# Kernel tuning notes

Hardware: AMD Instinct MI355X
Metric: run time of the kernel (lower is better)

The kernel has to match this reference:

```python
import jax, jax.numpy as jnp
import numpy as np

B, T, E, D, A = 32, 2048, 1024, 1024, 1024
SHARPENING = 1.0


def setup_inputs() -> dict:
    key = jax.random.key(0)
    ks = jax.random.split(key, 8)
    s = 0.02
    return {
        "enc_out": jax.random.normal(ks[0], (B, T, E), jnp.float32),
        "x_lens": jax.random.randint(ks[1], (B,), 1, T + 1, jnp.int32),
        "dec_out": jax.random.normal(ks[2], (B, 1, D), jnp.float32),
        "att_weights_step": jax.random.uniform(ks[3], (B, T), jnp.float32),
        "W_enc": jax.random.normal(ks[4], (E, A), jnp.float32) * s,
        "b_enc": jnp.zeros((A,), jnp.float32),
        "W_dec": jax.random.normal(ks[5], (D, A), jnp.float32) * s,
        "v": jax.random.normal(ks[6], (A,), jnp.float32) * s,
    }


def reference(enc_out, x_lens, dec_out, att_weights_step, W_enc, b_enc, W_dec, v):
    # content (Bahdanau additive) attention
    # energy[b,t] = v . tanh(W_enc enc[b,t] + b_enc + W_dec dec[b])
    enc_proj = jnp.einsum("bte,ea->bta", enc_out, W_enc) + b_enc  # [B,T,A]
    dec_proj = jnp.einsum("bod,da->boa", dec_out, W_dec)          # [B,1,A]
    energy = jnp.einsum("bta,a->bt", jnp.tanh(enc_proj + dec_proj), v)  # [B,T]
    # original multiplies energy by a 0/1 length mask (NOT -inf masking)
    mask = (jnp.arange(T)[None, :] < x_lens[:, None]).astype(energy.dtype)
    energy = energy * mask * SHARPENING
    att = jax.nn.softmax(energy, axis=-1)  # [B,T]
    context_vec = jnp.einsum("bte,bt->be", enc_out, att)[:, None, :]  # [B,1,E]
    return context_vec, att
```

## Files before the change

kernel.cpp:

```cpp
#include <hip/hip_runtime.h>
#include <hip/hip_bf16.h>
#include <stdint.h>


typedef __bf16 bf16;
typedef __bf16 bf16x8 __attribute__((ext_vector_type(8)));
typedef __bf16 bf16x4 __attribute__((ext_vector_type(4)));
typedef float floatx4 __attribute__((ext_vector_type(4)));

#define T_DIM 2048
#define B_DIM 32
#define K_DIM 1024
#define N_DIM 1024
#define M_DIM (B_DIM * T_DIM)
#define ENC_ELEMS ((size_t)M_DIM * K_DIM)

__device__ __forceinline__ void async_copy16(const bf16* g, bf16* l) {
    __builtin_amdgcn_global_load_lds(
        (const __attribute__((address_space(1))) void*)g,
        (__attribute__((address_space(3))) void*)l, 16, 0, 0);
}

__device__ __forceinline__ float fast_tanh(float x) {
    float ax = fabsf(x);
    float e  = __expf(ax + ax);
    float t  = 1.f - 2.f / (e + 1.f);
    return copysignf(t, x);
}

__global__ __launch_bounds__(256) void cvt_enc(const float* __restrict__ in,
                                               bf16* __restrict__ out) {
    size_t i = ((size_t)blockIdx.x * 256 + threadIdx.x) * 8;
    const size_t stride = (size_t)gridDim.x * 256 * 8;
    for (; i < ENC_ELEMS; i += stride) {
        float4 f0 = *(const float4*)(in + i);
        float4 f1 = *(const float4*)(in + i + 4);
        bf16x8 w;
        w[0] = (bf16)f0.x; w[1] = (bf16)f0.y; w[2] = (bf16)f0.z; w[3] = (bf16)f0.w;
        w[4] = (bf16)f1.x; w[5] = (bf16)f1.y; w[6] = (bf16)f1.z; w[7] = (bf16)f1.w;
        *(bf16x8*)(out + i) = w;
    }
}

__global__ __launch_bounds__(256) void transpose_wenc(
        const float* __restrict__ W, bf16* __restrict__ WT) {
    __shared__ bf16 tile[64][65];
    const int e0 = blockIdx.x * 64, a0 = blockIdx.y * 64;
    const int c = threadIdx.x & 63, r0 = threadIdx.x >> 6;
#pragma unroll
    for (int p = 0; p < 16; ++p) {
        int r = p * 4 + r0;
        tile[r][c] = (bf16)W[(size_t)(e0 + r) * 1024 + a0 + c];
    }
    __syncthreads();
#pragma unroll
    for (int p = 0; p < 16; ++p) {
        int r = p * 4 + r0;
        WT[(size_t)(a0 + r) * 1024 + e0 + c] = tile[c][r];
    }
}

__global__ __launch_bounds__(256) void decproj_kernel(
        const float* __restrict__ dec, const float* __restrict__ Wdec,
        const float* __restrict__ benc, float* __restrict__ dproj) {
    const int bg = blockIdx.x;
    const int a0 = blockIdx.y * 64;
    const int al = threadIdx.x & 63;
    const int dq = threadIdx.x >> 6;
    const int a  = a0 + al;
    __shared__ float sdec[8][1024];
    for (int i = threadIdx.x; i < 8192; i += 256)
        sdec[i >> 10][i & 1023] = dec[bg * 8192 + i];
    __syncthreads();
    float acc[8];
#pragma unroll
    for (int b = 0; b < 8; ++b) acc[b] = 0.f;
    for (int d = dq * 256; d < dq * 256 + 256; ++d) {
        const float w = Wdec[(size_t)d * 1024 + a];
#pragma unroll
        for (int b = 0; b < 8; ++b) acc[b] += sdec[b][d] * w;
    }
    __shared__ float red[4][8][64];
#pragma unroll
    for (int b = 0; b < 8; ++b) red[dq][b][al] = acc[b];
    __syncthreads();
    if (dq == 0) {
        const float be = benc[a];
#pragma unroll
        for (int b = 0; b < 8; ++b)
            dproj[(bg * 8 + b) * 1024 + a] =
                be + red[0][b][al] + red[1][b][al] + red[2][b][al] + red[3][b][al];
    }
}


#define HT 8192

#define BARRIER()  __builtin_amdgcn_s_barrier()
#define SCHEDB()   __builtin_amdgcn_sched_barrier(0)
#define VMCNT(n)   asm volatile("s_waitcnt vmcnt(" #n ")")

#define STAGE_A(kt, h, sl) {                                                   \
    const bf16* g_ = encb + (size_t)(m0 + (h)*128 + wave*8 + (lane>>3)) * 1024 \
                     + (kt)*64 + srccol;                                       \
    bf16* l_ = As + (((sl)*2 + (h)) * HT) + wave * 512;                        \
    async_copy16(g_, l_);                                                      \
    async_copy16(g_ + (size_t)64*1024, l_ + 4096);                             \
}
#define STAGE_B(kt, h) {                                                       \
    const bf16* g_ = WT + (size_t)(n0 + (h)*128 + wave*8 + (lane>>3)) * 1024   \
                     + (kt)*64 + srccol;                                       \
    bf16* l_ = Bs + ((((kt)&1)*2 + (h)) * HT) + wave * 512;                    \
    async_copy16(g_, l_);                                                      \
    async_copy16(g_ + (size_t)64*1024, l_ + 4096);                             \
}

__global__ __launch_bounds__(512, 2) void energy_gemm_8ph(
        const bf16* __restrict__ encb, const bf16* __restrict__ WT,
        const float* __restrict__ dproj, const float* __restrict__ v,
        float* __restrict__ part) {
    __shared__ __align__(16) bf16 As[6 * HT];
    __shared__ __align__(16) bf16 Bs[4 * HT];
    float* esum = (float*)As;

    const int tid  = threadIdx.x;
    const int lane = tid & 63;
    const int wave = tid >> 6;
    const int wm   = wave >> 2;
    const int wn   = wave & 3;
    const int lo   = lane & 15;
    const int hi   = lane >> 4;

    const int L = blockIdx.x;
    const int xcd  = L & 7;
    const int slot = L >> 3;
    const int m_tile  = xcd * 32 + (slot >> 2);
    const int n_chunk = slot & 3;
    const int m0 = m_tile * 256;
    const int n0 = n_chunk * 256;
    const int b  = m0 >> 11;

    const int srccol = (((lane & 7) ^ (lane >> 3)) << 3);
    const int swz0 = ((hi)     ^ (lo & 7)) << 3;
    const int swz1 = ((4 | hi) ^ (lo & 7)) << 3;

    floatx4 acc[2][2][4][2];
#pragma unroll
    for (int a_ = 0; a_ < 2; ++a_)
#pragma unroll
      for (int b_ = 0; b_ < 2; ++b_)
#pragma unroll
        for (int c_ = 0; c_ < 4; ++c_)
#pragma unroll
          for (int d_ = 0; d_ < 2; ++d_)
            acc[a_][b_][c_][d_] = (floatx4){0.f, 0.f, 0.f, 0.f};

    float vv[2][2], dp[2][2];
#pragma unroll
    for (int qn = 0; qn < 2; ++qn)
#pragma unroll
      for (int nf = 0; nf < 2; ++nf) {
        int col = n0 + qn * 128 + wn * 32 + nf * 16 + lo;
        vv[qn][nf] = v[col];
        dp[qn][nf] = dproj[b * 1024 + col];
      }
    SCHEDB();
    VMCNT(0);
    SCHEDB();

    STAGE_B(0, 0); STAGE_B(0, 1);
    STAGE_A(0, 0, 0); STAGE_A(0, 1, 0);
    STAGE_A(1, 0, 1); STAGE_A(1, 1, 1);
    SCHEDB();
    VMCNT(4);
    SCHEDB();
    BARRIER();

    int aslot = 0;
#pragma unroll 1
    for (int t = 0; t < 16; ++t) {
        const int tb   = t & 1;
        const int asl2 = (aslot >= 1) ? (aslot - 1) : 2;
        const bf16* Bh0 = Bs + (tb * 2 + 0) * HT;
        const bf16* Bh1 = Bs + (tb * 2 + 1) * HT;
        const bf16* Ah0 = As + (aslot * 2 + 0) * HT;
        const bf16* Ah1 = As + (aslot * 2 + 1) * HT;

        bf16x8 bfr[2][2][2], af0[4][2], af1[4][2];
#pragma unroll
        for (int qn = 0; qn < 2; ++qn) {
            const bf16* Bh_ = qn ? Bh1 : Bh0;
#pragma unroll
            for (int nf = 0; nf < 2; ++nf) {
                bfr[qn][nf][0] = *(const bf16x8*)(Bh_ + (wn*32 + nf*16 + lo)*64 + swz0);
                bfr[qn][nf][1] = *(const bf16x8*)(Bh_ + (wn*32 + nf*16 + lo)*64 + swz1);
            }
        }
#pragma unroll
        for (int mf = 0; mf < 4; ++mf) {
            af0[mf][0] = *(const bf16x8*)(Ah0 + (wm*64 + mf*16 + lo)*64 + swz0);
            af0[mf][1] = *(const bf16x8*)(Ah0 + (wm*64 + mf*16 + lo)*64 + swz1);
        }
        if (t < 15) { STAGE_B(t + 1, 0); STAGE_B(t + 1, 1); }

        __builtin_amdgcn_s_setprio(1);
#pragma unroll
        for (int kk = 0; kk < 2; ++kk)
#pragma unroll
          for (int mf = 0; mf < 4; ++mf)
#pragma unroll
            for (int qn = 0; qn < 2; ++qn)
#pragma unroll
              for (int nf = 0; nf < 2; ++nf)
                acc[0][qn][mf][nf] = __builtin_amdgcn_mfma_f32_16x16x32_bf16(
                    af0[mf][kk], bfr[qn][nf][kk], acc[0][qn][mf][nf], 0, 0, 0);
        __builtin_amdgcn_s_setprio(0);

#pragma unroll
        for (int mf = 0; mf < 4; ++mf) {
            af1[mf][0] = *(const bf16x8*)(Ah1 + (wm*64 + mf*16 + lo)*64 + swz0);
            af1[mf][1] = *(const bf16x8*)(Ah1 + (wm*64 + mf*16 + lo)*64 + swz1);
        }
        if (t < 14) { STAGE_A(t + 2, 0, asl2); STAGE_A(t + 2, 1, asl2); }

        __builtin_amdgcn_s_setprio(1);
#pragma unroll
        for (int kk = 0; kk < 2; ++kk)
#pragma unroll
          for (int mf = 0; mf < 4; ++mf)
#pragma unroll
            for (int qn = 0; qn < 2; ++qn)
#pragma unroll
              for (int nf = 0; nf < 2; ++nf)
                acc[1][qn][mf][nf] = __builtin_amdgcn_mfma_f32_16x16x32_bf16(
                    af1[mf][kk], bfr[qn][nf][kk], acc[1][qn][mf][nf], 0, 0, 0);
        __builtin_amdgcn_s_setprio(0);

        SCHEDB();
        if (t < 14) { VMCNT(4); } else if (t == 14) { VMCNT(0); }
        SCHEDB();
        BARRIER();
        aslot = (aslot == 2) ? 0 : aslot + 1;
    }

    __syncthreads();
#pragma unroll
    for (int qm = 0; qm < 2; ++qm)
#pragma unroll
      for (int mf = 0; mf < 4; ++mf)
#pragma unroll
        for (int r = 0; r < 4; ++r) {
          float s = 0.f;
#pragma unroll
          for (int qn = 0; qn < 2; ++qn)
#pragma unroll
            for (int nf = 0; nf < 2; ++nf)
              s += vv[qn][nf] * fast_tanh(acc[qm][qn][mf][nf][r] + dp[qn][nf]);
          s += __shfl_xor(s, 1);
          s += __shfl_xor(s, 2);
          s += __shfl_xor(s, 4);
          s += __shfl_xor(s, 8);
          if (lo == 0)
            esum[wn * 256 + qm * 128 + wm * 64 + mf * 16 + hi * 4 + r] = s;
        }
    __syncthreads();
    if (tid < 256)
        part[(size_t)n_chunk * M_DIM + m0 + tid] =
            esum[tid] + esum[256 + tid] + esum[512 + tid] + esum[768 + tid];
}

__global__ __launch_bounds__(256) void energy_gemm_f32(
        const float* __restrict__ enc, const bf16* __restrict__ WT,
        const float* __restrict__ dproj, const float* __restrict__ v,
        float* __restrict__ part) {
    __shared__ __align__(16) bf16 As[128 * 32];
    __shared__ __align__(16) bf16 Bs[128 * 32];
    __shared__ float esum[128];

    const int tid  = threadIdx.x;
    const int lane = tid & 63;
    const int wave = tid >> 6;
    const int wy = wave >> 1, wx = wave & 1;
    const int L = blockIdx.x;
    const int xcd  = L & 7;
    const int slot = L >> 3;
    const int m_tile = xcd * 64 + (slot >> 3);
    const int n_chunk = slot & 7;
    const int m0 = m_tile * 128;
    const int n0 = n_chunk * 128;
    const int b  = m0 >> 11;

    if (tid < 128) esum[tid] = 0.f;

    floatx4 acc[4][4];
#pragma unroll
    for (int i = 0; i < 4; ++i)
#pragma unroll
        for (int j = 0; j < 4; ++j) acc[i][j] = (floatx4){0.f, 0.f, 0.f, 0.f};

    const int sr = tid >> 2;
    const int sc = (tid & 3) * 8;
    const float* gA = enc + (size_t)(m0 + sr) * 1024 + sc;
    const bf16*  gB = WT  + (size_t)(n0 + sr) * 1024 + sc;
    bf16* lA = As + sr * 32 + sc;
    bf16* lB = Bs + sr * 32 + sc;

    for (int k0 = 0; k0 < K_DIM; k0 += 32) {
        __syncthreads();
#pragma unroll
        for (int rep = 0; rep < 2; ++rep) {
            const float4* p = (const float4*)(gA + (size_t)rep * 64 * 1024 + k0);
            float4 f0 = p[0], f1 = p[1];
            bf16x8 w;
            w[0] = (bf16)f0.x; w[1] = (bf16)f0.y; w[2] = (bf16)f0.z; w[3] = (bf16)f0.w;
            w[4] = (bf16)f1.x; w[5] = (bf16)f1.y; w[6] = (bf16)f1.z; w[7] = (bf16)f1.w;
            *(bf16x8*)(lA + rep * 64 * 32) = w;
            *(bf16x8*)(lB + rep * 64 * 32) =
                *(const bf16x8*)(gB + (size_t)rep * 64 * 1024 + k0);
        }
        __syncthreads();

        bf16x8 af[4], bfrg[4];
#pragma unroll
        for (int i = 0; i < 4; ++i)
            af[i] = *(const bf16x8*)(As + (wy * 64 + i * 16 + (lane & 15)) * 32 + (lane >> 4) * 8);
#pragma unroll
        for (int i = 0; i < 4; ++i)
            bfrg[i] = *(const bf16x8*)(Bs + (wx * 64 + i * 16 + (lane & 15)) * 32 + (lane >> 4) * 8);
#pragma unroll
        for (int mi = 0; mi < 4; ++mi)
#pragma unroll
            for (int ni = 0; ni < 4; ++ni)
                acc[mi][ni] = __builtin_amdgcn_mfma_f32_16x16x32_bf16(
                    af[mi], bfrg[ni], acc[mi][ni], 0, 0, 0);
    }
    __syncthreads();

    float vv[4], dp[4];
#pragma unroll
    for (int ni = 0; ni < 4; ++ni) {
        int col = n0 + wx * 64 + ni * 16 + (lane & 15);
        vv[ni] = v[col];
        dp[ni] = dproj[b * 1024 + col];
    }
#pragma unroll
    for (int mi = 0; mi < 4; ++mi) {
#pragma unroll
        for (int r = 0; r < 4; ++r) {
            float s = 0.f;
#pragma unroll
            for (int ni = 0; ni < 4; ++ni)
                s += vv[ni] * fast_tanh(acc[mi][ni][r] + dp[ni]);
            s += __shfl_xor(s, 1);
            s += __shfl_xor(s, 2);
            s += __shfl_xor(s, 4);
            s += __shfl_xor(s, 8);
            if ((lane & 15) == 0) {
                int row = wy * 64 + mi * 16 + (lane >> 4) * 4 + r;
                atomicAdd(&esum[row], s);
            }
        }
    }
    __syncthreads();
    if (tid < 128) part[(size_t)n_chunk * M_DIM + m0 + tid] = esum[tid];
}

__global__ __launch_bounds__(256) void softmax_kernel(
        const float* __restrict__ part, const int* __restrict__ xlens,
        float* __restrict__ att, int nc) {
    const int b = blockIdx.x, tid = threadIdx.x;
    const int len = xlens[b];
    float e[8];
    float mx = -3.4e38f;
#pragma unroll
    for (int i = 0; i < 8; ++i) {
        const int t = tid + i * 256;
        float s = 0.f;
#pragma unroll 4
        for (int c = 0; c < nc; ++c) s += part[(size_t)c * M_DIM + b * 2048 + t];
        e[i] = (t < len) ? s : 0.f;
        mx = fmaxf(mx, e[i]);
    }
#pragma unroll
    for (int off = 1; off < 64; off <<= 1) mx = fmaxf(mx, __shfl_xor(mx, off));
    __shared__ float sr1[4], sr2[4];
    if ((tid & 63) == 0) sr1[tid >> 6] = mx;
    __syncthreads();
    mx = fmaxf(fmaxf(sr1[0], sr1[1]), fmaxf(sr1[2], sr1[3]));
    float sum = 0.f;
#pragma unroll
    for (int i = 0; i < 8; ++i) { e[i] = __expf(e[i] - mx); sum += e[i]; }
#pragma unroll
    for (int off = 1; off < 64; off <<= 1) sum += __shfl_xor(sum, off);
    if ((tid & 63) == 0) sr2[tid >> 6] = sum;
    __syncthreads();
    sum = sr2[0] + sr2[1] + sr2[2] + sr2[3];
    const float inv = 1.f / sum;
#pragma unroll
    for (int i = 0; i < 8; ++i)
        att[b * 2048 + tid + i * 256] = e[i] * inv;
}

__global__ __launch_bounds__(256) void context_part_kernel(
        const bf16* __restrict__ encb, const float* __restrict__ att,
        float* __restrict__ ctxpart) {
    const int b = blockIdx.x, chunk = blockIdx.y, tid = threadIdx.x;
    const int t0 = chunk * 128;
    __shared__ float satt[128];
    if (tid < 128) satt[tid] = att[b * 2048 + t0 + tid];
    __syncthreads();
    const bf16* base = encb + ((size_t)b * 2048 + t0) * 1024 + tid * 4;
    float a0 = 0.f, a1 = 0.f, a2 = 0.f, a3 = 0.f;
#pragma unroll 4
    for (int t = 0; t < 128; ++t) {
        bf16x4 ev = *(const bf16x4*)(base + (size_t)t * 1024);
        float w = satt[t];
        a0 += w * (float)ev[0]; a1 += w * (float)ev[1];
        a2 += w * (float)ev[2]; a3 += w * (float)ev[3];
    }
    float* o = ctxpart + ((size_t)b * 16 + chunk) * 1024 + tid * 4;
    o[0] = a0; o[1] = a1; o[2] = a2; o[3] = a3;
}

__global__ __launch_bounds__(256) void context_reduce_kernel(
        const float* __restrict__ ctxpart, float* __restrict__ out_ctx) {
    const int i = blockIdx.x * 256 + threadIdx.x;
    const int b = i >> 10, e = i & 1023;
    const float* p = ctxpart + (size_t)b * 16 * 1024 + e;
    float s = 0.f;
#pragma unroll
    for (int c = 0; c < 16; ++c) s += p[c * 1024];
    out_ctx[i] = s;
}

__global__ __launch_bounds__(256) void context_kernel_f32(
        const float* __restrict__ enc, const float* __restrict__ att,
        float* __restrict__ ctx) {
    const int b = blockIdx.x, t0 = blockIdx.y * 128, tid = threadIdx.x;
    __shared__ float satt[128];
    if (tid < 128) satt[tid] = att[b * 2048 + t0 + tid];
    __syncthreads();
    const float* base = enc + ((size_t)b * 2048 + t0) * 1024 + tid * 4;
    float a0 = 0.f, a1 = 0.f, a2 = 0.f, a3 = 0.f;
    for (int t = 0; t < 128; ++t) {
        float4 ev = *(const float4*)(base + (size_t)t * 1024);
        float w = satt[t];
        a0 += w * ev.x; a1 += w * ev.y; a2 += w * ev.z; a3 += w * ev.w;
    }
    float* o = ctx + b * 1024 + tid * 4;
    atomicAdd(o + 0, a0); atomicAdd(o + 1, a1);
    atomicAdd(o + 2, a2); atomicAdd(o + 3, a3);
}

extern "C" void kernel_launch(void* const* d_in, const int* in_sizes, int n_in,
                              void* d_out, int out_size, void* d_ws, size_t ws_size,
                              hipStream_t stream) {
    const float* enc   = (const float*)d_in[0];
    const int*   xlens = (const int*)d_in[1];
    const float* dec   = (const float*)d_in[2];
    const float* Wenc  = (const float*)d_in[4];
    const float* benc  = (const float*)d_in[5];
    const float* Wdec  = (const float*)d_in[6];
    const float* v     = (const float*)d_in[7];

    float* out_ctx = (float*)d_out;
    float* out_att = out_ctx + B_DIM * K_DIM;

    char* ws = (char*)d_ws;
    float* dproj   = (float*)ws;
    bf16*  WT      = (bf16*)(ws + (128u << 10));
    float* part    = (float*)(ws + (128u << 10) + (2u << 20));
    bf16*  encb    = (bf16*)(ws + (128u << 10) + (4u << 20));
    float* ctxpart = (float*)(ws + (128u << 10) + (4u << 20) + (ENC_ELEMS * 2));
    const size_t need = (128u << 10) + (4u << 20) + ENC_ELEMS * 2 + (2u << 21);

    transpose_wenc<<<dim3(16, 16), 256, 0, stream>>>(Wenc, WT);
    decproj_kernel<<<dim3(4, 16), 256, 0, stream>>>(dec, Wdec, benc, dproj);

    if (ws_size >= need) {
        cvt_enc<<<2048, 256, 0, stream>>>(enc, encb);
        energy_gemm_8ph<<<1024, 512, 0, stream>>>(encb, WT, dproj, v, part);
        softmax_kernel<<<B_DIM, 256, 0, stream>>>(part, xlens, out_att, 4);
        context_part_kernel<<<dim3(B_DIM, 16), 256, 0, stream>>>(encb, out_att, ctxpart);
        context_reduce_kernel<<<B_DIM * K_DIM / 256, 256, 0, stream>>>(ctxpart, out_ctx);
    } else {
        hipMemsetAsync(out_ctx, 0, B_DIM * K_DIM * sizeof(float), stream);
        energy_gemm_f32<<<4096, 256, 0, stream>>>(enc, WT, dproj, v, part);
        softmax_kernel<<<B_DIM, 256, 0, stream>>>(part, xlens, out_att, 8);
        context_kernel_f32<<<dim3(B_DIM, 16), 256, 0, stream>>>(enc, out_att, out_ctx);
    }
}
```

Measured before the change: 582.2 us.

## Fuse fp32-to-bf16 conversion of encoder into GEMM A-tile staging

```diff
diff --git a/kernel.cpp b/kernel.cpp
--- a/kernel.cpp
+++ b/kernel.cpp
@@ -5,7 +5,6 @@
 
 typedef __bf16 bf16;
 typedef __bf16 bf16x8 __attribute__((ext_vector_type(8)));
-typedef __bf16 bf16x4 __attribute__((ext_vector_type(4)));
 typedef float floatx4 __attribute__((ext_vector_type(4)));
 
 #define T_DIM 2048
@@ -13,7 +12,6 @@
 #define K_DIM 1024
 #define N_DIM 1024
 #define M_DIM (B_DIM * T_DIM)
-#define ENC_ELEMS ((size_t)M_DIM * K_DIM)
 
 __device__ __forceinline__ void async_copy16(const bf16* g, bf16* l) {
     __builtin_amdgcn_global_load_lds(
@@ -26,20 +24,6 @@
     float e  = __expf(ax + ax);
     float t  = 1.f - 2.f / (e + 1.f);
     return copysignf(t, x);
-}
-
-__global__ __launch_bounds__(256) void cvt_enc(const float* __restrict__ in,
-                                               bf16* __restrict__ out) {
-    size_t i = ((size_t)blockIdx.x * 256 + threadIdx.x) * 8;
-    const size_t stride = (size_t)gridDim.x * 256 * 8;
-    for (; i < ENC_ELEMS; i += stride) {
-        float4 f0 = *(const float4*)(in + i);
-        float4 f1 = *(const float4*)(in + i + 4);
-        bf16x8 w;
-        w[0] = (bf16)f0.x; w[1] = (bf16)f0.y; w[2] = (bf16)f0.z; w[3] = (bf16)f0.w;
-        w[4] = (bf16)f1.x; w[5] = (bf16)f1.y; w[6] = (bf16)f1.z; w[7] = (bf16)f1.w;
-        *(bf16x8*)(out + i) = w;
-    }
 }
 
 __global__ __launch_bounds__(256) void transpose_wenc(
@@ -99,14 +83,8 @@
 #define BARRIER()  __builtin_amdgcn_s_barrier()
 #define SCHEDB()   __builtin_amdgcn_sched_barrier(0)
 #define VMCNT(n)   asm volatile("s_waitcnt vmcnt(" #n ")")
-
-#define STAGE_A(kt, h, sl) {                                                   \
-    const bf16* g_ = encb + (size_t)(m0 + (h)*128 + wave*8 + (lane>>3)) * 1024 \
-                     + (kt)*64 + srccol;                                       \
-    bf16* l_ = As + (((sl)*2 + (h)) * HT) + wave * 512;                        \
-    async_copy16(g_, l_);                                                      \
-    async_copy16(g_ + (size_t)64*1024, l_ + 4096);                             \
-}
+#define LGKM0()    asm volatile("s_waitcnt lgkmcnt(0)")
+
 #define STAGE_B(kt, h) {                                                       \
     const bf16* g_ = WT + (size_t)(n0 + (h)*128 + wave*8 + (lane>>3)) * 1024   \
                      + (kt)*64 + srccol;                                       \
@@ -115,11 +93,31 @@
     async_copy16(g_ + (size_t)64*1024, l_ + 4096);                             \
 }
 
-__global__ __launch_bounds__(512, 2) void energy_gemm_8ph(
-        const bf16* __restrict__ encb, const bf16* __restrict__ WT,
+#define LOAD_A(kt, h, q0, q1, q2, q3) {                                        \
+    const float* g_ = enc + (size_t)(m0 + (h)*128 + row0) * 1024               \
+                      + (kt)*64 + cg * 8;                                      \
+    q0 = *(const float4*)g_;                                                   \
+    q1 = *(const float4*)(g_ + 4);                                             \
+    q2 = *(const float4*)(g_ + (size_t)64 * 1024);                             \
+    q3 = *(const float4*)(g_ + (size_t)64 * 1024 + 4);                         \
+}
+
+#define WRITE_A(sl, h, q0, q1, q2, q3) {                                       \
+    bf16x8 w0_, w1_;                                                           \
+    w0_[0]=(bf16)q0.x; w0_[1]=(bf16)q0.y; w0_[2]=(bf16)q0.z; w0_[3]=(bf16)q0.w;\
+    w0_[4]=(bf16)q1.x; w0_[5]=(bf16)q1.y; w0_[6]=(bf16)q1.z; w0_[7]=(bf16)q1.w;\
+    w1_[0]=(bf16)q2.x; w1_[1]=(bf16)q2.y; w1_[2]=(bf16)q2.z; w1_[3]=(bf16)q2.w;\
+    w1_[4]=(bf16)q3.x; w1_[5]=(bf16)q3.y; w1_[6]=(bf16)q3.z; w1_[7]=(bf16)q3.w;\
+    bf16* l_ = As + (((sl)*2 + (h)) * HT) + row0 * 64 + wslot * 8;             \
+    *(bf16x8*)(l_) = w0_;                                                      \
+    *(bf16x8*)(l_ + 4096) = w1_;                                  \
+}
+
+__global__ __launch_bounds__(512, 2) void energy_gemm_fused(
+        const float* __restrict__ enc, const bf16* __restrict__ WT,
         const float* __restrict__ dproj, const float* __restrict__ v,
         float* __restrict__ part) {
-    __shared__ __align__(16) bf16 As[6 * HT];
+    __shared__ __align__(16) bf16 As[4 * HT];
     __shared__ __align__(16) bf16 Bs[4 * HT];
     float* esum = (float*)As;
 
@@ -140,7 +138,10 @@
     const int n0 = n_chunk * 256;
     const int b  = m0 >> 11;
 
-    const int srccol = (((lane & 7) ^ (lane >> 3)) << 3);
+    const int row0  = wave * 8 + (lane >> 3);
+    const int cg    = lane & 7;
+    const int wslot = cg ^ (lane >> 3);
+    const int srccol = wslot << 3;
     const int swz0 = ((hi)     ^ (lo & 7)) << 3;
     const int swz1 = ((4 | hi) ^ (lo & 7)) << 3;
 
@@ -164,27 +165,31 @@
         vv[qn][nf] = v[col];
         dp[qn][nf] = dproj[b * 1024 + col];
       }
+
+    {
+        float4 p0, p1, p2, p3, r0, r1, r2, r3;
+        LOAD_A(0, 0, p0, p1, p2, p3);
+        LOAD_A(0, 1, r0, r1, r2, r3);
+        STAGE_B(0, 0); STAGE_B(0, 1);
+        WRITE_A(0, 0, p0, p1, p2, p3);
+        WRITE_A(0, 1, r0, r1, r2, r3);
+    }
     SCHEDB();
+    LGKM0();
     VMCNT(0);
     SCHEDB();
-
-    STAGE_B(0, 0); STAGE_B(0, 1);
-    STAGE_A(0, 0, 0); STAGE_A(0, 1, 0);
-    STAGE_A(1, 0, 1); STAGE_A(1, 1, 1);
-    SCHEDB();
-    VMCNT(4);
-    SCHEDB();
     BARRIER();
 
-    int aslot = 0;
 #pragma unroll 1
     for (int t = 0; t < 16; ++t) {
-        const int tb   = t & 1;
-        const int asl2 = (aslot >= 1) ? (aslot - 1) : 2;
-        const bf16* Bh0 = Bs + (tb * 2 + 0) * HT;
-        const bf16* Bh1 = Bs + (tb * 2 + 1) * HT;
-        const bf16* Ah0 = As + (aslot * 2 + 0) * HT;
-        const bf16* Ah1 = As + (aslot * 2 + 1) * HT;
+        const int cur = t & 1, nxt = cur ^ 1;
+        const bf16* Ah0 = As + (cur * 2 + 0) * HT;
+        const bf16* Ah1 = As + (cur * 2 + 1) * HT;
+        const bf16* Bh0 = Bs + (cur * 2 + 0) * HT;
+        const bf16* Bh1 = Bs + (cur * 2 + 1) * HT;
+
+        float4 qa0, qa1, qa2, qa3;
+        if (t < 15) { LOAD_A(t + 1, 0, qa0, qa1, qa2, qa3); }
 
         bf16x8 bfr[2][2][2], af0[4][2], af1[4][2];
 #pragma unroll
@@ -216,12 +221,17 @@
                     af0[mf][kk], bfr[qn][nf][kk], acc[0][qn][mf][nf], 0, 0, 0);
         __builtin_amdgcn_s_setprio(0);
 
+        float4 qb0, qb1, qb2, qb3;
+        if (t < 15) {
+            WRITE_A(nxt, 0, qa0, qa1, qa2, qa3);
+            LOAD_A(t + 1, 1, qb0, qb1, qb2, qb3);
+        }
+
 #pragma unroll
         for (int mf = 0; mf < 4; ++mf) {
             af1[mf][0] = *(const bf16x8*)(Ah1 + (wm*64 + mf*16 + lo)*64 + swz0);
             af1[mf][1] = *(const bf16x8*)(Ah1 + (wm*64 + mf*16 + lo)*64 + swz1);
         }
-        if (t < 14) { STAGE_A(t + 2, 0, asl2); STAGE_A(t + 2, 1, asl2); }
 
         __builtin_amdgcn_s_setprio(1);
 #pragma unroll
@@ -236,11 +246,13 @@
                     af1[mf][kk], bfr[qn][nf][kk], acc[1][qn][mf][nf], 0, 0, 0);
         __builtin_amdgcn_s_setprio(0);
 
+        if (t < 15) { WRITE_A(nxt, 1, qb0, qb1, qb2, qb3); }
+
         SCHEDB();
-        if (t < 14) { VMCNT(4); } else if (t == 14) { VMCNT(0); }
+        LGKM0();
+        VMCNT(0);
         SCHEDB();
         BARRIER();
-        aslot = (aslot == 2) ? 0 : aslot + 1;
     }
 
     __syncthreads();
@@ -401,22 +413,21 @@
         att[b * 2048 + tid + i * 256] = e[i] * inv;
 }
 
-__global__ __launch_bounds__(256) void context_part_kernel(
-        const bf16* __restrict__ encb, const float* __restrict__ att,
+__global__ __launch_bounds__(256) void context_part_f32(
+        const float* __restrict__ enc, const float* __restrict__ att,
         float* __restrict__ ctxpart) {
     const int b = blockIdx.x, chunk = blockIdx.y, tid = threadIdx.x;
     const int t0 = chunk * 128;
     __shared__ float satt[128];
     if (tid < 128) satt[tid] = att[b * 2048 + t0 + tid];
     __syncthreads();
-    const bf16* base = encb + ((size_t)b * 2048 + t0) * 1024 + tid * 4;
+    const float* base = enc + ((size_t)b * 2048 + t0) * 1024 + tid * 4;
     float a0 = 0.f, a1 = 0.f, a2 = 0.f, a3 = 0.f;
 #pragma unroll 4
     for (int t = 0; t < 128; ++t) {
-        bf16x4 ev = *(const bf16x4*)(base + (size_t)t * 1024);
+        float4 ev = *(const float4*)(base + (size_t)t * 1024);
         float w = satt[t];
-        a0 += w * (float)ev[0]; a1 += w * (float)ev[1];
-        a2 += w * (float)ev[2]; a3 += w * (float)ev[3];
+        a0 += w * ev.x; a1 += w * ev.y; a2 += w * ev.z; a3 += w * ev.w;
     }
     float* o = ctxpart + ((size_t)b * 16 + chunk) * 1024 + tid * 4;
     o[0] = a0; o[1] = a1; o[2] = a2; o[3] = a3;
@@ -470,18 +481,16 @@
     float* dproj   = (float*)ws;
     bf16*  WT      = (bf16*)(ws + (128u << 10));
     float* part    = (float*)(ws + (128u << 10) + (2u << 20));
-    bf16*  encb    = (bf16*)(ws + (128u << 10) + (4u << 20));
-    float* ctxpart = (float*)(ws + (128u << 10) + (4u << 20) + (ENC_ELEMS * 2));
-    const size_t need = (128u << 10) + (4u << 20) + ENC_ELEMS * 2 + (2u << 21);
+    float* ctxpart = (float*)(ws + (128u << 10) + (4u << 20));
+    const size_t need = (128u << 10) + (6u << 20);
 
     transpose_wenc<<<dim3(16, 16), 256, 0, stream>>>(Wenc, WT);
     decproj_kernel<<<dim3(4, 16), 256, 0, stream>>>(dec, Wdec, benc, dproj);
 
     if (ws_size >= need) {
-        cvt_enc<<<2048, 256, 0, stream>>>(enc, encb);
-        energy_gemm_8ph<<<1024, 512, 0, stream>>>(encb, WT, dproj, v, part);
+        energy_gemm_fused<<<1024, 512, 0, stream>>>(enc, WT, dproj, v, part);
         softmax_kernel<<<B_DIM, 256, 0, stream>>>(part, xlens, out_att, 4);
-        context_part_kernel<<<dim3(B_DIM, 16), 256, 0, stream>>>(encb, out_att, ctxpart);
+        context_part_f32<<<dim3(B_DIM, 16), 256, 0, stream>>>(enc, out_att, ctxpart);
         context_reduce_kernel<<<B_DIM * K_DIM / 256, 256, 0, stream>>>(ctxpart, out_ctx);
     } else {
         hipMemsetAsync(out_ctx, 0, B_DIM * K_DIM * sizeof(float), stream);
```

New measurement: 608.7 us. +4.5%, slower.

## Merge prep kernels into one launch and fuse softmax with context reduction

Applied to the files above, without the earlier changes.

```diff
diff --git a/kernel.cpp b/kernel.cpp
--- a/kernel.cpp
+++ b/kernel.cpp
@@ -28,68 +28,72 @@
     return copysignf(t, x);
 }
 
-__global__ __launch_bounds__(256) void cvt_enc(const float* __restrict__ in,
-                                               bf16* __restrict__ out) {
-    size_t i = ((size_t)blockIdx.x * 256 + threadIdx.x) * 8;
-    const size_t stride = (size_t)gridDim.x * 256 * 8;
-    for (; i < ENC_ELEMS; i += stride) {
-        float4 f0 = *(const float4*)(in + i);
-        float4 f1 = *(const float4*)(in + i + 4);
-        bf16x8 w;
-        w[0] = (bf16)f0.x; w[1] = (bf16)f0.y; w[2] = (bf16)f0.z; w[3] = (bf16)f0.w;
-        w[4] = (bf16)f1.x; w[5] = (bf16)f1.y; w[6] = (bf16)f1.z; w[7] = (bf16)f1.w;
-        *(bf16x8*)(out + i) = w;
-    }
-}
-
-__global__ __launch_bounds__(256) void transpose_wenc(
-        const float* __restrict__ W, bf16* __restrict__ WT) {
-    __shared__ bf16 tile[64][65];
-    const int e0 = blockIdx.x * 64, a0 = blockIdx.y * 64;
-    const int c = threadIdx.x & 63, r0 = threadIdx.x >> 6;
-#pragma unroll
-    for (int p = 0; p < 16; ++p) {
-        int r = p * 4 + r0;
-        tile[r][c] = (bf16)W[(size_t)(e0 + r) * 1024 + a0 + c];
-    }
-    __syncthreads();
-#pragma unroll
-    for (int p = 0; p < 16; ++p) {
-        int r = p * 4 + r0;
-        WT[(size_t)(a0 + r) * 1024 + e0 + c] = tile[c][r];
-    }
-}
-
-__global__ __launch_bounds__(256) void decproj_kernel(
+__global__ __launch_bounds__(256) void prep_kernel(
+        const float* __restrict__ W, bf16* __restrict__ WT,
         const float* __restrict__ dec, const float* __restrict__ Wdec,
-        const float* __restrict__ benc, float* __restrict__ dproj) {
-    const int bg = blockIdx.x;
-    const int a0 = blockIdx.y * 64;
-    const int al = threadIdx.x & 63;
-    const int dq = threadIdx.x >> 6;
-    const int a  = a0 + al;
-    __shared__ float sdec[8][1024];
-    for (int i = threadIdx.x; i < 8192; i += 256)
-        sdec[i >> 10][i & 1023] = dec[bg * 8192 + i];
-    __syncthreads();
-    float acc[8];
-#pragma unroll
-    for (int b = 0; b < 8; ++b) acc[b] = 0.f;
-    for (int d = dq * 256; d < dq * 256 + 256; ++d) {
-        const float w = Wdec[(size_t)d * 1024 + a];
-#pragma unroll
-        for (int b = 0; b < 8; ++b) acc[b] += sdec[b][d] * w;
-    }
-    __shared__ float red[4][8][64];
-#pragma unroll
-    for (int b = 0; b < 8; ++b) red[dq][b][al] = acc[b];
-    __syncthreads();
-    if (dq == 0) {
-        const float be = benc[a];
-#pragma unroll
-        for (int b = 0; b < 8; ++b)
-            dproj[(bg * 8 + b) * 1024 + a] =
-                be + red[0][b][al] + red[1][b][al] + red[2][b][al] + red[3][b][al];
+        const float* __restrict__ benc, float* __restrict__ dproj,
+        const float* __restrict__ enc, bf16* __restrict__ encb) {
+    __shared__ union {
+        bf16 tile[64][65];
+        struct { float sdec[8][1024]; float red[4][8][64]; } dp;
+    } sm;
+    const int bid = blockIdx.x;
+    const int tid = threadIdx.x;
+
+    if (bid < 256) {
+        const int e0 = (bid & 15) * 64, a0 = (bid >> 4) * 64;
+        const int c = tid & 63, r0 = tid >> 6;
+#pragma unroll
+        for (int p = 0; p < 16; ++p) {
+            int r = p * 4 + r0;
+            sm.tile[r][c] = (bf16)W[(size_t)(e0 + r) * 1024 + a0 + c];
+        }
+        __syncthreads();
+#pragma unroll
+        for (int p = 0; p < 16; ++p) {
+            int r = p * 4 + r0;
+            WT[(size_t)(a0 + r) * 1024 + e0 + c] = sm.tile[c][r];
+        }
+    } else if (bid < 320) {
+        const int bg = (bid - 256) >> 4;
+        const int a0 = ((bid - 256) & 15) * 64;
+        const int al = tid & 63;
+        const int dq = tid >> 6;
+        const int a  = a0 + al;
+        for (int i = tid; i < 8192; i += 256)
+            sm.dp.sdec[i >> 10][i & 1023] = dec[bg * 8192 + i];
+        __syncthreads();
+        float acc[8];
+#pragma unroll
+        for (int b = 0; b < 8; ++b) acc[b] = 0.f;
+        for (int d = dq * 256; d < dq * 256 + 256; ++d) {
+            const float w = Wdec[(size_t)d * 1024 + a];
+#pragma unroll
+            for (int b = 0; b < 8; ++b) acc[b] += sm.dp.sdec[b][d] * w;
+        }
+        __syncthreads();
+#pragma unroll
+        for (int b = 0; b < 8; ++b) sm.dp.red[dq][b][al] = acc[b];
+        __syncthreads();
+        if (dq == 0) {
+            const float be = benc[a];
+#pragma unroll
+            for (int b = 0; b < 8; ++b)
+                dproj[(bg * 8 + b) * 1024 + a] =
+                    be + sm.dp.red[0][b][al] + sm.dp.red[1][b][al] +
+                         sm.dp.red[2][b][al] + sm.dp.red[3][b][al];
+        }
+    } else {
+        size_t i = ((size_t)(bid - 320) * 256 + tid) * 8;
+        const size_t stride = (size_t)2048 * 256 * 8;
+        for (; i < ENC_ELEMS; i += stride) {
+            float4 f0 = *(const float4*)(enc + i);
+            float4 f1 = *(const float4*)(enc + i + 4);
+            bf16x8 w;
+            w[0] = (bf16)f0.x; w[1] = (bf16)f0.y; w[2] = (bf16)f0.z; w[3] = (bf16)f0.w;
+            w[4] = (bf16)f1.x; w[5] = (bf16)f1.y; w[6] = (bf16)f1.z; w[7] = (bf16)f1.w;
+            *(bf16x8*)(encb + i) = w;
+        }
     }
 }
 
@@ -269,12 +273,71 @@
             esum[tid] + esum[256 + tid] + esum[512 + tid] + esum[768 + tid];
 }
 
+__global__ __launch_bounds__(256) void softmax_context(
+        const float* __restrict__ part, const int* __restrict__ xlens,
+        const bf16* __restrict__ encb, float* __restrict__ att,
+        float* __restrict__ ctx) {
+    const int b = blockIdx.x, chunk = blockIdx.y, tid = threadIdx.x;
+    const int t0 = chunk * 128;
+    const int len = xlens[b];
+    __shared__ float se[2048];
+    __shared__ float sr1[4], sr2[4];
+    __shared__ float satt[128];
+
+    float e[8];
+    float mx = -3.4e38f;
+#pragma unroll
+    for (int i = 0; i < 8; ++i) {
+        const int t = tid + i * 256;
+        float s = 0.f;
+#pragma unroll
+        for (int c = 0; c < 4; ++c) s += part[(size_t)c * M_DIM + b * 2048 + t];
+        e[i] = (t < len) ? s : 0.f;
+        se[t] = e[i];
+        mx = fmaxf(mx, e[i]);
+    }
+#pragma unroll
+    for (int off = 1; off < 64; off <<= 1) mx = fmaxf(mx, __shfl_xor(mx, off));
+    if ((tid & 63) == 0) sr1[tid >> 6] = mx;
+    __syncthreads();
+    mx = fmaxf(fmaxf(sr1[0], sr1[1]), fmaxf(sr1[2], sr1[3]));
+    float sum = 0.f;
+#pragma unroll
+    for (int i = 0; i < 8; ++i) sum += __expf(e[i] - mx);
+#pragma unroll
+    for (int off = 1; off < 64; off <<= 1) sum += __shfl_xor(sum, off);
+    if ((tid & 63) == 0) sr2[tid >> 6] = sum;
+    __syncthreads();
+    sum = sr2[0] + sr2[1] + sr2[2] + sr2[3];
+    const float inv = 1.f / sum;
+
+    if (tid < 128) {
+        float a = __expf(se[t0 + tid] - mx) * inv;
+        satt[tid] = a;
+        att[b * 2048 + t0 + tid] = a;
+    }
+    __syncthreads();
+
+    const bf16* base = encb + ((size_t)b * 2048 + t0) * 1024 + tid * 4;
+    float a0 = 0.f, a1 = 0.f, a2 = 0.f, a3 = 0.f;
+#pragma unroll 4
+    for (int t = 0; t < 128; ++t) {
+        bf16x4 ev = *(const bf16x4*)(base + (size_t)t * 1024);
+        float w = satt[t];
+        a0 += w * (float)ev[0]; a1 += w * (float)ev[1];
+        a2 += w * (float)ev[2]; a3 += w * (float)ev[3];
+    }
+    float* o = ctx + b * 1024 + tid * 4;
+    atomicAdd(o + 0, a0); atomicAdd(o + 1, a1);
+    atomicAdd(o + 2, a2); atomicAdd(o + 3, a3);
+}
+
 __global__ __launch_bounds__(256) void energy_gemm_f32(
         const float* __restrict__ enc, const bf16* __restrict__ WT,
         const float* __restrict__ dproj, const float* __restrict__ v,
         float* __restrict__ part) {
-    __shared__ __align__(16) bf16 As[128 * 32];
-    __shared__ __align__(16) bf16 Bs[128 * 32];
+    __shared__ __align__(16) bf16 Asf[128 * 32];
+    __shared__ __align__(16) bf16 Bsf[128 * 32];
     __shared__ float esum[128];
 
     const int tid  = threadIdx.x;
@@ -302,8 +365,8 @@
     const int sc = (tid & 3) * 8;
     const float* gA = enc + (size_t)(m0 + sr) * 1024 + sc;
     const bf16*  gB = WT  + (size_t)(n0 + sr) * 1024 + sc;
-    bf16* lA = As + sr * 32 + sc;
-    bf16* lB = Bs + sr * 32 + sc;
+    bf16* lA = Asf + sr * 32 + sc;
+    bf16* lB = Bsf + sr * 32 + sc;
 
     for (int k0 = 0; k0 < K_DIM; k0 += 32) {
         __syncthreads();
@@ -323,10 +386,10 @@
         bf16x8 af[4], bfrg[4];
 #pragma unroll
         for (int i = 0; i < 4; ++i)
-            af[i] = *(const bf16x8*)(As + (wy * 64 + i * 16 + (lane & 15)) * 32 + (lane >> 4) * 8);
+            af[i] = *(const bf16x8*)(Asf + (wy * 64 + i * 16 + (lane & 15)) * 32 + (lane >> 4) * 8);
 #pragma unroll
         for (int i = 0; i < 4; ++i)
-            bfrg[i] = *(const bf16x8*)(Bs + (wx * 64 + i * 16 + (lane & 15)) * 32 + (lane >> 4) * 8);
+            bfrg[i] = *(const bf16x8*)(Bsf + (wx * 64 + i * 16 + (lane & 15)) * 32 + (lane >> 4) * 8);
 #pragma unroll
         for (int mi = 0; mi < 4; ++mi)
 #pragma unroll
@@ -401,36 +464,55 @@
         att[b * 2048 + tid + i * 256] = e[i] * inv;
 }
 
-__global__ __launch_bounds__(256) void context_part_kernel(
-        const bf16* __restrict__ encb, const float* __restrict__ att,
-        float* __restrict__ ctxpart) {
-    const int b = blockIdx.x, chunk = blockIdx.y, tid = threadIdx.x;
-    const int t0 = chunk * 128;
-    __shared__ float satt[128];
-    if (tid < 128) satt[tid] = att[b * 2048 + t0 + tid];
-    __syncthreads();
-    const bf16* base = encb + ((size_t)b * 2048 + t0) * 1024 + tid * 4;
-    float a0 = 0.f, a1 = 0.f, a2 = 0.f, a3 = 0.f;
-#pragma unroll 4
-    for (int t = 0; t < 128; ++t) {
-        bf16x4 ev = *(const bf16x4*)(base + (size_t)t * 1024);
-        float w = satt[t];
-        a0 += w * (float)ev[0]; a1 += w * (float)ev[1];
-        a2 += w * (float)ev[2]; a3 += w * (float)ev[3];
-    }
-    float* o = ctxpart + ((size_t)b * 16 + chunk) * 1024 + tid * 4;
-    o[0] = a0; o[1] = a1; o[2] = a2; o[3] = a3;
-}
-
-__global__ __launch_bounds__(256) void context_reduce_kernel(
-        const float* __restrict__ ctxpart, float* __restrict__ out_ctx) {
-    const int i = blockIdx.x * 256 + threadIdx.x;
-    const int b = i >> 10, e = i & 1023;
-    const float* p = ctxpart + (size_t)b * 16 * 1024 + e;
-    float s = 0.f;
-#pragma unroll
-    for (int c = 0; c < 16; ++c) s += p[c * 1024];
-    out_ctx[i] = s;
+__global__ __launch_bounds__(256) void transpose_wenc(
+        const float* __restrict__ W, bf16* __restrict__ WT) {
+    __shared__ bf16 tile[64][65];
+    const int e0 = blockIdx.x * 64, a0 = blockIdx.y * 64;
+    const int c = threadIdx.x & 63, r0 = threadIdx.x >> 6;
+#pragma unroll
+    for (int p = 0; p < 16; ++p) {
+        int r = p * 4 + r0;
+        tile[r][c] = (bf16)W[(size_t)(e0 + r) * 1024 + a0 + c];
+    }
+    __syncthreads();
+#pragma unroll
+    for (int p = 0; p < 16; ++p) {
+        int r = p * 4 + r0;
+        WT[(size_t)(a0 + r) * 1024 + e0 + c] = tile[c][r];
+    }
+}
+
+__global__ __launch_bounds__(256) void decproj_kernel(
+        const float* __restrict__ dec, const float* __restrict__ Wdec,
+        const float* __restrict__ benc, float* __restrict__ dproj) {
+    const int bg = blockIdx.x;
+    const int a0 = blockIdx.y * 64;
+    const int al = threadIdx.x & 63;
+    const int dq = threadIdx.x >> 6;
+    const int a  = a0 + al;
+    __shared__ float sdec[8][1024];
+    for (int i = threadIdx.x; i < 8192; i += 256)
+        sdec[i >> 10][i & 1023] = dec[bg * 8192 + i];
+    __syncthreads();
+    float acc[8];
+#pragma unroll
+    for (int b = 0; b < 8; ++b) acc[b] = 0.f;
+    for (int d = dq * 256; d < dq * 256 + 256; ++d) {
+        const float w = Wdec[(size_t)d * 1024 + a];
+#pragma unroll
+        for (int b = 0; b < 8; ++b) acc[b] += sdec[b][d] * w;
+    }
+    __shared__ float red[4][8][64];
+#pragma unroll
+    for (int b = 0; b < 8; ++b) red[dq][b][al] = acc[b];
+    __syncthreads();
+    if (dq == 0) {
+        const float be = benc[a];
+#pragma unroll
+        for (int b = 0; b < 8; ++b)
+            dproj[(bg * 8 + b) * 1024 + a] =
+                be + red[0][b][al] + red[1][b][al] + red[2][b][al] + red[3][b][al];
+    }
 }
 
 __global__ __launch_bounds__(256) void context_kernel_f32(
@@ -467,23 +549,22 @@
     float* out_att = out_ctx + B_DIM * K_DIM;
 
     char* ws = (char*)d_ws;
-    float* dproj   = (float*)ws;
-    bf16*  WT      = (bf16*)(ws + (128u << 10));
-    float* part    = (float*)(ws + (128u << 10) + (2u << 20));
-    bf16*  encb    = (bf16*)(ws + (128u << 10) + (4u << 20));
-    float* ctxpart = (float*)(ws + (128u << 10) + (4u << 20) + (ENC_ELEMS * 2));
-    const size_t need = (128u << 10) + (4u << 20) + ENC_ELEMS * 2 + (2u << 21);
-
-    transpose_wenc<<<dim3(16, 16), 256, 0, stream>>>(Wenc, WT);
-    decproj_kernel<<<dim3(4, 16), 256, 0, stream>>>(dec, Wdec, benc, dproj);
+    float* dproj = (float*)ws;
+    bf16*  WT    = (bf16*)(ws + (128u << 10));
+    float* part  = (float*)(ws + (128u << 10) + (2u << 20));
+    bf16*  encb  = (bf16*)(ws + (128u << 10) + (4u << 20));
+    const size_t need = (128u << 10) + (4u << 20) + ENC_ELEMS * 2;
 
     if (ws_size >= need) {
-        cvt_enc<<<2048, 256, 0, stream>>>(enc, encb);
+        prep_kernel<<<2368, 256, 0, stream>>>(Wenc, WT, dec, Wdec, benc, dproj,
+                                              enc, encb);
         energy_gemm_8ph<<<1024, 512, 0, stream>>>(encb, WT, dproj, v, part);
-        softmax_kernel<<<B_DIM, 256, 0, stream>>>(part, xlens, out_att, 4);
-        context_part_kernel<<<dim3(B_DIM, 16), 256, 0, stream>>>(encb, out_att, ctxpart);
-        context_reduce_kernel<<<B_DIM * K_DIM / 256, 256, 0, stream>>>(ctxpart, out_ctx);
+        hipMemsetAsync(out_ctx, 0, B_DIM * K_DIM * sizeof(float), stream);
+        softmax_context<<<dim3(B_DIM, 16), 256, 0, stream>>>(part, xlens, encb,
+                                                             out_att, out_ctx);
     } else {
+        transpose_wenc<<<dim3(16, 16), 256, 0, stream>>>(Wenc, WT);
+        decproj_kernel<<<dim3(4, 16), 256, 0, stream>>>(dec, Wdec, benc, dproj);
         hipMemsetAsync(out_ctx, 0, B_DIM * K_DIM * sizeof(float), stream);
         energy_gemm_f32<<<4096, 256, 0, stream>>>(enc, WT, dproj, v, part);
         softmax_kernel<<<B_DIM, 256, 0, stream>>>(part, xlens, out_att, 8);
```

Result: faster. 562.7 us (-3.4%).
